# Kernel optimization log

Hardware: AMD Instinct MI355X
Metric: run time of the kernel (lower is better)

The kernel has to match this reference:

```python
import jax, jax.numpy as jnp
import numpy as np

DUNITS = 1024
ATT_DIM = 1024
EPROJ = 1024
T = 16384
SCALING = 2.0


def setup_inputs() -> dict:
    key = jax.random.key(0)
    ks = jax.random.split(key, 8)
    dec_z = jax.random.normal(ks[0], (1, DUNITS), dtype=jnp.float32)
    att_prev = jnp.zeros((1, T), dtype=jnp.float32)
    pre_compute_enc_h = jax.random.normal(ks[1], (1, T, ATT_DIM), dtype=jnp.float32)
    enc_h = jax.random.normal(ks[2], (1, T, EPROJ), dtype=jnp.float32)
    mask = jnp.zeros((1, T), dtype=jnp.float32)
    # learned params: mlp_dec Linear(dunits->att_dim), gvec Linear(att_dim->1)
    W_dec = jax.random.normal(ks[3], (DUNITS, ATT_DIM), dtype=jnp.float32) / np.sqrt(DUNITS)
    b_dec = jnp.zeros((ATT_DIM,), dtype=jnp.float32)
    w_gvec = jax.random.normal(ks[4], (ATT_DIM,), dtype=jnp.float32) / np.sqrt(ATT_DIM)
    b_gvec = jnp.zeros((), dtype=jnp.float32)
    return {
        "dec_z": dec_z,
        "att_prev": att_prev,
        "pre_compute_enc_h": pre_compute_enc_h,
        "enc_h": enc_h,
        "mask": mask,
        "W_dec": W_dec,
        "b_dec": b_dec,
        "w_gvec": w_gvec,
        "b_gvec": b_gvec,
    }


def reference(dec_z, att_prev, pre_compute_enc_h, enc_h, mask, W_dec, b_dec, w_gvec, b_gvec):
    # dec_z: [1, dunits] -> mlp_dec -> [1, 1, att_dim]
    dec_z_tiled = (dec_z @ W_dec + b_dec)[:, None, :]
    # gvec(tanh(pre + tile)).squeeze(2): [1, T]
    e = jnp.einsum("bta,a->bt", jnp.tanh(pre_compute_enc_h + dec_z_tiled), w_gvec) + b_gvec
    e = e + mask
    w = jax.nn.softmax(SCALING * e, axis=1)  # [1, T]
    c = jnp.einsum("bte,bt->be", enc_h, w)   # [1, eproj]
    return (c, w)
```

## Files before the change

### kernel.cpp

```cpp
#include <hip/hip_runtime.h>
#include <math.h>

#define TT   16384
#define ADIM 1024
#define NCH  1024
#define RPW  4
#define NCH2 64

__device__ __forceinline__ float ftanh(float x) {
    float e2 = __expf(2.0f * x);
    return 1.0f - 2.0f * __builtin_amdgcn_rcpf(e2 + 1.0f);
}

__global__ void k1_gemv_part(const float* __restrict__ z, const float* __restrict__ W,
                             float* __restrict__ part) {
    int b = blockIdx.x, tid = threadIdx.x;
    float4 acc = {0.f, 0.f, 0.f, 0.f};
#pragma unroll
    for (int i = 0; i < 4; ++i) {
        int d = b * 4 + i;
        float zv = z[d];
        float4 w4 = reinterpret_cast<const float4*>(W)[(size_t)d * 256 + tid];
        acc.x += zv * w4.x; acc.y += zv * w4.y; acc.z += zv * w4.z; acc.w += zv * w4.w;
    }
    reinterpret_cast<float4*>(part)[(size_t)b * 256 + tid] = acc;
}

__global__ void k2_gemv_red(const float* __restrict__ part, const float* __restrict__ bdec,
                            float* __restrict__ dp) {
    int b = blockIdx.x, tid = threadIdx.x;
    int lane = tid & 63, wv = tid >> 6;
    int rsub = lane >> 2;
    int colg = lane & 3;
    float4 acc = {0.f, 0.f, 0.f, 0.f};
#pragma unroll
    for (int i = 0; i < 4; ++i) {
        int row = i * 64 + wv * 16 + rsub;
        float4 v = reinterpret_cast<const float4*>(part)[(size_t)row * 256 + b * 4 + colg];
        acc.x += v.x; acc.y += v.y; acc.z += v.z; acc.w += v.w;
    }
#pragma unroll
    for (int off = 4; off <= 32; off <<= 1) {
        acc.x += __shfl_xor(acc.x, off, 64);
        acc.y += __shfl_xor(acc.y, off, 64);
        acc.z += __shfl_xor(acc.z, off, 64);
        acc.w += __shfl_xor(acc.w, off, 64);
    }
    __shared__ float4 lds[4][4];
    if (lane < 4) lds[wv][lane] = acc;
    __syncthreads();
    if (tid < 4) {
        float4 t = {0.f, 0.f, 0.f, 0.f};
#pragma unroll
        for (int w = 0; w < 4; ++w) {
            float4 v = lds[w][tid];
            t.x += v.x; t.y += v.y; t.z += v.z; t.w += v.w;
        }
        float4 bd = reinterpret_cast<const float4*>(bdec)[b * 4 + tid];
        t.x += bd.x; t.y += bd.y; t.z += bd.z; t.w += bd.w;
        reinterpret_cast<float4*>(dp)[b * 4 + tid] = t;
    }
}

__global__ void __launch_bounds__(256) k3_fused(
    const float* __restrict__ pre, const float* __restrict__ enc,
    const float* __restrict__ dp, const float* __restrict__ wg,
    const float* __restrict__ bgp, const float* __restrict__ mask,
    float* __restrict__ e_out, float* __restrict__ m_out,
    float* __restrict__ s_out, float* __restrict__ cpart) {
    int b = blockIdx.x, tid = threadIdx.x;
    int lane = tid & 63, wv = tid >> 6;
    float4 d4[4], g4[4];
    const float4* dp4 = reinterpret_cast<const float4*>(dp);
    const float4* wg4 = reinterpret_cast<const float4*>(wg);
#pragma unroll
    for (int j = 0; j < 4; ++j) { d4[j] = dp4[j * 64 + lane]; g4[j] = wg4[j * 64 + lane]; }
    float bgv = bgp[0];
    int t0 = b * (4 * RPW) + wv * RPW;

    float et[RPW];
#pragma unroll
    for (int i = 0; i < RPW; ++i) {
        const float4* pr = reinterpret_cast<const float4*>(pre) + (size_t)(t0 + i) * 256;
        float dot = 0.f;
#pragma unroll
        for (int j = 0; j < 4; ++j) {
            float4 p = pr[j * 64 + lane];
            dot += ftanh(p.x + d4[j].x) * g4[j].x;
            dot += ftanh(p.y + d4[j].y) * g4[j].y;
            dot += ftanh(p.z + d4[j].z) * g4[j].z;
            dot += ftanh(p.w + d4[j].w) * g4[j].w;
        }
        et[i] = dot;
    }
#pragma unroll
    for (int i = 0; i < RPW; ++i) {
#pragma unroll
        for (int off = 32; off; off >>= 1) et[i] += __shfl_xor(et[i], off, 64);
        et[i] = 2.0f * (et[i] + bgv + mask[t0 + i]);
    }
    if (lane == 0) {
#pragma unroll
        for (int i = 0; i < RPW; ++i) e_out[t0 + i] = et[i];
    }

    float m = et[0];
#pragma unroll
    for (int i = 1; i < RPW; ++i) m = fmaxf(m, et[i]);
    float p[RPW], s = 0.f;
#pragma unroll
    for (int i = 0; i < RPW; ++i) { p[i] = __expf(et[i] - m); s += p[i]; }

    float4 ca[4] = {{0,0,0,0},{0,0,0,0},{0,0,0,0},{0,0,0,0}};
#pragma unroll
    for (int i = 0; i < RPW; ++i) {
        const float4* er = reinterpret_cast<const float4*>(enc) + (size_t)(t0 + i) * 256;
#pragma unroll
        for (int j = 0; j < 4; ++j) {
            float4 v = er[j * 64 + lane];
            ca[j].x += p[i] * v.x; ca[j].y += p[i] * v.y;
            ca[j].z += p[i] * v.z; ca[j].w += p[i] * v.w;
        }
    }

    __shared__ float lm[4], ls[4];
    __shared__ float4 lc[4][256];
#pragma unroll
    for (int j = 0; j < 4; ++j) lc[wv][j * 64 + lane] = ca[j];
    if (lane == 0) { lm[wv] = m; ls[wv] = s; }
    __syncthreads();
    float Mb = fmaxf(fmaxf(lm[0], lm[1]), fmaxf(lm[2], lm[3]));
    float s0 = __expf(lm[0] - Mb), s1 = __expf(lm[1] - Mb);
    float s2 = __expf(lm[2] - Mb), s3 = __expf(lm[3] - Mb);
    if (tid == 0) {
        m_out[b] = Mb;
        s_out[b] = ls[0] * s0 + ls[1] * s1 + ls[2] * s2 + ls[3] * s3;
    }
    float4 v0 = lc[0][tid], v1 = lc[1][tid], v2 = lc[2][tid], v3 = lc[3][tid];
    float4 o;
    o.x = v0.x * s0 + v1.x * s1 + v2.x * s2 + v3.x * s3;
    o.y = v0.y * s0 + v1.y * s1 + v2.y * s2 + v3.y * s3;
    o.z = v0.z * s0 + v1.z * s1 + v2.z * s2 + v3.z * s3;
    o.w = v0.w * s0 + v1.w * s1 + v2.w * s2 + v3.w * s3;
    reinterpret_cast<float4*>(cpart)[(size_t)b * 256 + tid] = o;
}

__global__ void __launch_bounds__(256) k4_fold(
    const float* __restrict__ m_arr, const float* __restrict__ s_arr,
    const float* __restrict__ cpart, float* __restrict__ cpart2,
    float* __restrict__ msout) {
    int b = blockIdx.x, tid = threadIdx.x;
    int lane = tid & 63, wv = tid >> 6;
    __shared__ float redm[4], reds[4];
    float mloc = -3.0e38f;
#pragma unroll
    for (int i = 0; i < NCH / 256; ++i) mloc = fmaxf(mloc, m_arr[tid + i * 256]);
#pragma unroll
    for (int off = 32; off; off >>= 1) mloc = fmaxf(mloc, __shfl_xor(mloc, off, 64));
    if (lane == 0) redm[wv] = mloc;
    __syncthreads();
    float M = fmaxf(fmaxf(redm[0], redm[1]), fmaxf(redm[2], redm[3]));
    float4 acc = {0.f, 0.f, 0.f, 0.f};
#pragma unroll
    for (int i = 0; i < NCH / NCH2; ++i) {
        int r = b * (NCH / NCH2) + i;
        float sc = __expf(m_arr[r] - M);
        float4 v = reinterpret_cast<const float4*>(cpart)[(size_t)r * 256 + tid];
        acc.x += sc * v.x; acc.y += sc * v.y; acc.z += sc * v.z; acc.w += sc * v.w;
    }
    reinterpret_cast<float4*>(cpart2)[(size_t)b * 256 + tid] = acc;
    if (b == 0) {
        float sl = 0.f;
#pragma unroll
        for (int i = 0; i < NCH / 256; ++i)
            sl += s_arr[tid + i * 256] * __expf(m_arr[tid + i * 256] - M);
#pragma unroll
        for (int off = 32; off; off >>= 1) sl += __shfl_xor(sl, off, 64);
        if (lane == 0) reds[wv] = sl;
        __syncthreads();
        if (tid == 0) {
            float S = reds[0] + reds[1] + reds[2] + reds[3];
            msout[0] = M;
            msout[1] = 1.0f / S;
        }
    }
}

__global__ void __launch_bounds__(256) k5_final(
    const float* __restrict__ cpart2, const float* __restrict__ e,
    const float* __restrict__ ms, float* __restrict__ c_out,
    float* __restrict__ w_out) {
    int b = blockIdx.x, tid = threadIdx.x;
    float M = ms[0], invS = ms[1];
    if (b < 16) {
        int rs = tid >> 4;
        int cg = tid & 15;
        float4 acc = {0.f, 0.f, 0.f, 0.f};
#pragma unroll
        for (int i = 0; i < 4; ++i) {
            int r = rs * 4 + i;
            float4 v = reinterpret_cast<const float4*>(cpart2)[(size_t)r * 256 + b * 16 + cg];
            acc.x += v.x; acc.y += v.y; acc.z += v.z; acc.w += v.w;
        }
        __shared__ float4 lds[16][16];
        lds[rs][cg] = acc;
        __syncthreads();
        if (tid < 16) {
            float4 t = {0.f, 0.f, 0.f, 0.f};
#pragma unroll
            for (int r = 0; r < 16; ++r) {
                float4 v = lds[r][tid];
                t.x += v.x; t.y += v.y; t.z += v.z; t.w += v.w;
            }
            t.x *= invS; t.y *= invS; t.z *= invS; t.w *= invS;
            reinterpret_cast<float4*>(c_out)[b * 16 + tid] = t;
        }
    } else {
        int base = (b - 16) * 256 + tid;
        float4 ev = reinterpret_cast<const float4*>(e)[base];
        float4 w;
        w.x = __expf(ev.x - M) * invS;
        w.y = __expf(ev.y - M) * invS;
        w.z = __expf(ev.z - M) * invS;
        w.w = __expf(ev.w - M) * invS;
        reinterpret_cast<float4*>(w_out)[base] = w;
    }
}

extern "C" void kernel_launch(void* const* d_in, const int* in_sizes, int n_in,
                              void* d_out, int out_size, void* d_ws, size_t ws_size,
                              hipStream_t stream) {
    const float* dec_z = (const float*)d_in[0];
    const float* pre   = (const float*)d_in[2];
    const float* enc   = (const float*)d_in[3];
    const float* mask  = (const float*)d_in[4];
    const float* W_dec = (const float*)d_in[5];
    const float* b_dec = (const float*)d_in[6];
    const float* wg    = (const float*)d_in[7];
    const float* bg    = (const float*)d_in[8];

    float* out   = (float*)d_out;
    float* c_out = out;
    float* w_out = out + ADIM;

    float* ws = (float*)d_ws;
    float* part   = ws;
    float* dp     = part + 256 * ADIM;
    float* e_sc   = dp + ADIM;
    float* m_arr  = e_sc + TT;
    float* s_arr  = m_arr + NCH;
    float* cpart  = s_arr + NCH;
    float* cpart2 = cpart + (size_t)NCH * ADIM;
    float* ms     = cpart2 + (size_t)NCH2 * ADIM;

    k1_gemv_part<<<256, 256, 0, stream>>>(dec_z, W_dec, part);
    k2_gemv_red<<<64, 256, 0, stream>>>(part, b_dec, dp);
    k3_fused<<<NCH, 256, 0, stream>>>(pre, enc, dp, wg, bg, mask,
                                      e_sc, m_arr, s_arr, cpart);
    k4_fold<<<NCH2, 256, 0, stream>>>(m_arr, s_arr, cpart, cpart2, ms);
    k5_final<<<32, 256, 0, stream>>>(cpart2, e_sc, ms, c_out, w_out);
}
```

Before: 41.25 us.

## Split k3 work by column per wave, 8 rows per block, 2048 chunks

The fused score/context kernel now gives each wave a 256-column slice of the same 8 rows instead of 4 whole rows per wave. Row dot products are combined across waves through shared memory, which removes the per-block LDS merge of context partials. Loads are software-pipelined with two float4 buffers. The grid doubles to 2048 blocks, so the fold kernel reads twice as many partial context rows, and the larger cpart buffer adds memory traffic.

Result: faster. 40.11 us (-2.8%).

```diff
diff --git a/kernel.cpp b/kernel.cpp
--- a/kernel.cpp
+++ b/kernel.cpp
@@ -3,13 +3,18 @@
 
 #define TT   16384
 #define ADIM 1024
-#define NCH  1024
-#define RPW  4
+#define NCH  2048
+#define RPB  8
 #define NCH2 64
 
 __device__ __forceinline__ float ftanh(float x) {
     float e2 = __expf(2.0f * x);
     return 1.0f - 2.0f * __builtin_amdgcn_rcpf(e2 + 1.0f);
+}
+
+__device__ __forceinline__ float pdot(float4 p, float4 d, float4 g) {
+    return ftanh(p.x + d.x) * g.x + ftanh(p.y + d.y) * g.y +
+           ftanh(p.z + d.z) * g.z + ftanh(p.w + d.w) * g.w;
 }
 
 __global__ void k1_gemv_part(const float* __restrict__ z, const float* __restrict__ W,
@@ -61,6 +66,10 @@
         reinterpret_cast<float4*>(dp)[b * 4 + tid] = t;
     }
 }
+
+#define ACC(E, PW) do { \
+    ca.x += (PW) * (E).x; ca.y += (PW) * (E).y; \
+    ca.z += (PW) * (E).z; ca.w += (PW) * (E).w; } while (0)
 
 __global__ void __launch_bounds__(256) k3_fused(
     const float* __restrict__ pre, const float* __restrict__ enc,
@@ -70,79 +79,67 @@
     float* __restrict__ s_out, float* __restrict__ cpart) {
     int b = blockIdx.x, tid = threadIdx.x;
     int lane = tid & 63, wv = tid >> 6;
-    float4 d4[4], g4[4];
-    const float4* dp4 = reinterpret_cast<const float4*>(dp);
-    const float4* wg4 = reinterpret_cast<const float4*>(wg);
-#pragma unroll
-    for (int j = 0; j < 4; ++j) { d4[j] = dp4[j * 64 + lane]; g4[j] = wg4[j * 64 + lane]; }
+    int col = wv * 64 + lane;
+    float4 d4 = reinterpret_cast<const float4*>(dp)[col];
+    float4 g4 = reinterpret_cast<const float4*>(wg)[col];
     float bgv = bgp[0];
-    int t0 = b * (4 * RPW) + wv * RPW;
-
-    float et[RPW];
-#pragma unroll
-    for (int i = 0; i < RPW; ++i) {
-        const float4* pr = reinterpret_cast<const float4*>(pre) + (size_t)(t0 + i) * 256;
-        float dot = 0.f;
-#pragma unroll
-        for (int j = 0; j < 4; ++j) {
-            float4 p = pr[j * 64 + lane];
-            dot += ftanh(p.x + d4[j].x) * g4[j].x;
-            dot += ftanh(p.y + d4[j].y) * g4[j].y;
-            dot += ftanh(p.z + d4[j].z) * g4[j].z;
-            dot += ftanh(p.w + d4[j].w) * g4[j].w;
-        }
-        et[i] = dot;
-    }
-#pragma unroll
-    for (int i = 0; i < RPW; ++i) {
-#pragma unroll
-        for (int off = 32; off; off >>= 1) et[i] += __shfl_xor(et[i], off, 64);
-        et[i] = 2.0f * (et[i] + bgv + mask[t0 + i]);
-    }
+    int t0 = b * RPB;
+    const float4* pb = reinterpret_cast<const float4*>(pre) + (size_t)t0 * 256 + col;
+    const float4* eb = reinterpret_cast<const float4*>(enc) + (size_t)t0 * 256 + col;
+
+    float dt[RPB];
+    {
+        float4 B0 = pb[0], B1 = pb[256];
+        dt[0] = pdot(B0, d4, g4); B0 = pb[512];
+        dt[1] = pdot(B1, d4, g4); B1 = pb[768];
+        dt[2] = pdot(B0, d4, g4); B0 = pb[1024];
+        dt[3] = pdot(B1, d4, g4); B1 = pb[1280];
+        dt[4] = pdot(B0, d4, g4); B0 = pb[1536];
+        dt[5] = pdot(B1, d4, g4); B1 = pb[1792];
+        dt[6] = pdot(B0, d4, g4);
+        dt[7] = pdot(B1, d4, g4);
+    }
+#pragma unroll
+    for (int r = 0; r < RPB; ++r) {
+#pragma unroll
+        for (int off = 32; off; off >>= 1) dt[r] += __shfl_xor(dt[r], off, 64);
+    }
+    __shared__ float sd[4][RPB];
     if (lane == 0) {
 #pragma unroll
-        for (int i = 0; i < RPW; ++i) e_out[t0 + i] = et[i];
+        for (int r = 0; r < RPB; ++r) sd[wv][r] = dt[r];
+    }
+    __syncthreads();
+    float et[RPB];
+#pragma unroll
+    for (int r = 0; r < RPB; ++r)
+        et[r] = 2.0f * (sd[0][r] + sd[1][r] + sd[2][r] + sd[3][r] + bgv + mask[t0 + r]);
+    if (tid == 0) {
+#pragma unroll
+        for (int r = 0; r < RPB; ++r) e_out[t0 + r] = et[r];
     }
 
     float m = et[0];
 #pragma unroll
-    for (int i = 1; i < RPW; ++i) m = fmaxf(m, et[i]);
-    float p[RPW], s = 0.f;
-#pragma unroll
-    for (int i = 0; i < RPW; ++i) { p[i] = __expf(et[i] - m); s += p[i]; }
-
-    float4 ca[4] = {{0,0,0,0},{0,0,0,0},{0,0,0,0},{0,0,0,0}};
-#pragma unroll
-    for (int i = 0; i < RPW; ++i) {
-        const float4* er = reinterpret_cast<const float4*>(enc) + (size_t)(t0 + i) * 256;
-#pragma unroll
-        for (int j = 0; j < 4; ++j) {
-            float4 v = er[j * 64 + lane];
-            ca[j].x += p[i] * v.x; ca[j].y += p[i] * v.y;
-            ca[j].z += p[i] * v.z; ca[j].w += p[i] * v.w;
-        }
-    }
-
-    __shared__ float lm[4], ls[4];
-    __shared__ float4 lc[4][256];
-#pragma unroll
-    for (int j = 0; j < 4; ++j) lc[wv][j * 64 + lane] = ca[j];
-    if (lane == 0) { lm[wv] = m; ls[wv] = s; }
-    __syncthreads();
-    float Mb = fmaxf(fmaxf(lm[0], lm[1]), fmaxf(lm[2], lm[3]));
-    float s0 = __expf(lm[0] - Mb), s1 = __expf(lm[1] - Mb);
-    float s2 = __expf(lm[2] - Mb), s3 = __expf(lm[3] - Mb);
-    if (tid == 0) {
-        m_out[b] = Mb;
-        s_out[b] = ls[0] * s0 + ls[1] * s1 + ls[2] * s2 + ls[3] * s3;
-    }
-    float4 v0 = lc[0][tid], v1 = lc[1][tid], v2 = lc[2][tid], v3 = lc[3][tid];
-    float4 o;
-    o.x = v0.x * s0 + v1.x * s1 + v2.x * s2 + v3.x * s3;
-    o.y = v0.y * s0 + v1.y * s1 + v2.y * s2 + v3.y * s3;
-    o.z = v0.z * s0 + v1.z * s1 + v2.z * s2 + v3.z * s3;
-    o.w = v0.w * s0 + v1.w * s1 + v2.w * s2 + v3.w * s3;
-    reinterpret_cast<float4*>(cpart)[(size_t)b * 256 + tid] = o;
+    for (int r = 1; r < RPB; ++r) m = fmaxf(m, et[r]);
+    float p[RPB], s = 0.f;
+#pragma unroll
+    for (int r = 0; r < RPB; ++r) { p[r] = __expf(et[r] - m); s += p[r]; }
+    if (tid == 0) { m_out[b] = m; s_out[b] = s; }
+
+    float4 ca = {0.f, 0.f, 0.f, 0.f};
+    {
+        float4 E0 = eb[0], E1 = eb[256];
+        ACC(E0, p[0]); E0 = eb[512];
+        ACC(E1, p[1]); E1 = eb[768];
+        ACC(E0, p[2]); E0 = eb[1024];
+        ACC(E1, p[3]); E1 = eb[1280];
+        ACC(E0, p[4]); E0 = eb[1536];
+        ACC(E1, p[5]); E1 = eb[1792];
+        ACC(E0, p[6]);
+        ACC(E1, p[7]);
+    }
+    reinterpret_cast<float4*>(cpart)[(size_t)b * 256 + col] = ca;
 }
 
 __global__ void __launch_bounds__(256) k4_fold(
@@ -164,9 +161,9 @@
 #pragma unroll
     for (int i = 0; i < NCH / NCH2; ++i) {
         int r = b * (NCH / NCH2) + i;
-        float sc = __expf(m_arr[r] - M);
+        float scf = __expf(m_arr[r] - M);
         float4 v = reinterpret_cast<const float4*>(cpart)[(size_t)r * 256 + tid];
-        acc.x += sc * v.x; acc.y += sc * v.y; acc.z += sc * v.z; acc.w += sc * v.w;
+        acc.x += scf * v.x; acc.y += scf * v.y; acc.z += scf * v.z; acc.w += scf * v.w;
     }
     reinterpret_cast<float4*>(cpart2)[(size_t)b * 256 + tid] = acc;
     if (b == 0) {
```
